# Performance work log

Measured on AMD Instinct MI355X. Metric: run time of the kernel, lower is better.

## Reference

```python
import jax, jax.numpy as jnp
import numpy as np

B, MBS, F, CD = 512, 32768, 512, 16  # batch, mini_batch_size, filter_length, cond_dim

def setup_inputs() -> dict:
    key = jax.random.key(0)
    ks = jax.random.split(key, 8)
    return {
        "inputs": jax.random.normal(ks[0], (B, MBS, 1), jnp.float32),
        "c": jax.random.normal(ks[1], (B, 1, CD), jnp.float32),
        "W0": jax.random.normal(ks[2], (CD, F), jnp.float32) * 0.1,
        "b0": jnp.zeros((F,), jnp.float32),
        "alpha": jnp.full((F,), 0.25, jnp.float32),
        "Wg": jax.random.normal(ks[3], (CD, F), jnp.float32) * 0.1,
        "bg": jnp.zeros((F,), jnp.float32),
        "Wb": jax.random.normal(ks[4], (CD, F), jnp.float32) * 0.1,
        "bb": jnp.zeros((F,), jnp.float32),
        "Wglu": jax.random.normal(ks[5], (F, 2 * F), jnp.float32) * 0.05,
        "bglu": jnp.zeros((2 * F,), jnp.float32),
        "Wf": jax.random.normal(ks[6], (F, F), jnp.float32) * 0.05,
        "bf": jnp.zeros((F,), jnp.float32),
    }

def reference(inputs, c, W0, b0, alpha, Wg, bg, Wb, bb, Wglu, bglu, Wf, bf):
    mbs = inputs.shape[1]
    flen = Wf.shape[1]
    # conditioning stack: Dense -> PReLU -> FiLM -> GLU -> Dense(softsign)
    c_ = c @ W0 + b0                                  # [B,1,F]
    c_ = jnp.where(c_ >= 0, c_, alpha * c_)           # PReLU
    c_ = c_ * (c @ Wg + bg) + (c @ Wb + bb)           # FiLM
    g = c_ @ Wglu + bglu                              # [B,1,2F]
    a, gate = jnp.split(g, 2, axis=-1)
    c_ = a * jax.nn.sigmoid(gate)                     # GLU
    filters = jax.nn.soft_sign(c_ @ Wf + bf)          # [B,1,F]
    # FFT-based circular (linear via zero pad) convolution
    conv_len = mbs + flen - 1
    X = jnp.fft.fft(inputs[:, :, 0].astype(jnp.complex64), n=conv_len)   # [B,conv_len]
    H = jnp.fft.fft(filters[:, 0, :].astype(jnp.complex64), n=conv_len)  # [B,conv_len]
    y = jnp.fft.ifft(X * H)
    return jnp.real(y[:, :mbs])                       # [B,MBS]
```

## Files before the change

### kernel.cpp

```cpp
#include <hip/hip_runtime.h>


typedef float f32x16 __attribute__((ext_vector_type(16)));
typedef float f32x4  __attribute__((ext_vector_type(4)));
typedef __bf16 bf16x8 __attribute__((ext_vector_type(8)));

__device__ __forceinline__ unsigned short f2bf(float f) {
    unsigned int u = __float_as_uint(f);
    u += 0x7FFFu + ((u >> 16) & 1u);
    return (unsigned short)(u >> 16);
}

__device__ __forceinline__ uint4 pack8n(float4 a, float4 b) {
    bf16x8 v;
    v[0] = (__bf16)a.x; v[1] = (__bf16)a.y; v[2] = (__bf16)a.z; v[3] = (__bf16)a.w;
    v[4] = (__bf16)b.x; v[5] = (__bf16)b.y; v[6] = (__bf16)b.z; v[7] = (__bf16)b.w;
    uint4 r;
    __builtin_memcpy(&r, &v, 16);
    return r;
}

__global__ __launch_bounds__(256) void kA(
    const float* __restrict__ Wglu, const float* __restrict__ Wf,
    const float* __restrict__ c, const float* __restrict__ W0,
    const float* __restrict__ b0, const float* __restrict__ alpha,
    const float* __restrict__ Wg, const float* __restrict__ bg,
    const float* __restrict__ Wb, const float* __restrict__ bb,
    unsigned short* __restrict__ WgluT, unsigned short* __restrict__ WfT,
    unsigned short* __restrict__ cfilm) {
    const int blk = blockIdx.x, tid = threadIdx.x;
    if (blk < 192) {
        __shared__ float ldsF[64 * 65];
        const float* src; unsigned short* dst; int tj, tk, srcld;
        if (blk < 128) { tj = blk >> 3; tk = blk & 7; src = Wglu; dst = WgluT; srcld = 1024; }
        else { int b2 = blk - 128; tj = b2 >> 3; tk = b2 & 7; src = Wf; dst = WfT; srcld = 512; }
#pragma unroll
        for (int rr = 0; rr < 16; ++rr) {
            int kl = (tid >> 6) + (rr << 2), jl = tid & 63;
            ldsF[kl * 65 + jl] = src[(size_t)(tk * 64 + kl) * srcld + tj * 64 + jl];
        }
        __syncthreads();
#pragma unroll
        for (int rr = 0; rr < 16; ++rr) {
            int jl = (tid >> 6) + (rr << 2), kl = tid & 63;
            dst[(size_t)(tj * 64 + jl) * 512 + tk * 64 + kl] = f2bf(ldsF[kl * 65 + jl]);
        }
    } else {
        int id = (blk - 192) * 256 + tid;
        int b = id >> 9, f = id & 511;
        const float* cb = c + b * 16;
        float d0 = 0.f, dg = 0.f, db = 0.f;
#pragma unroll
        for (int i = 0; i < 16; ++i) {
            float cv = cb[i];
            d0 += cv * W0[i * 512 + f];
            dg += cv * Wg[i * 512 + f];
            db += cv * Wb[i * 512 + f];
        }
        float pre = d0 + b0[f];
        float pr = pre >= 0.f ? pre : alpha[f] * pre;
        float v = pr * (dg + bg[f]) + (db + bb[f]);
        cfilm[id] = f2bf(v);
    }
}

__global__ __launch_bounds__(256) void k2_glu(
    const unsigned short* __restrict__ cfilm, const unsigned short* __restrict__ WgluT,
    const float* __restrict__ bglu, unsigned short* __restrict__ cglu) {
    int wid = (blockIdx.x * 256 + threadIdx.x) >> 6;
    int l = threadIdx.x & 63;
    int tm = wid >> 5, tn = wid & 31;
    int row = tm * 16 + (l & 15);
    int col = tn * 16 + (l & 15);
    int kh = 8 * (l >> 4);
    f32x4 accA, accG;
#pragma unroll
    for (int i = 0; i < 4; ++i) { accA[i] = 0.f; accG[i] = 0.f; }
    const unsigned short* ap  = cfilm + row * 512 + kh;
    const unsigned short* bap = WgluT + col * 512 + kh;
    const unsigned short* bgp = WgluT + (512 + col) * 512 + kh;
#pragma unroll
    for (int kc = 0; kc < 16; ++kc) {
        bf16x8 a   = *(const bf16x8*)(ap  + kc * 32);
        bf16x8 ba  = *(const bf16x8*)(bap + kc * 32);
        bf16x8 bgt = *(const bf16x8*)(bgp + kc * 32);
        accA = __builtin_amdgcn_mfma_f32_16x16x32_bf16(a, ba,  accA, 0, 0, 0);
        accG = __builtin_amdgcn_mfma_f32_16x16x32_bf16(a, bgt, accG, 0, 0, 0);
    }
    float biasA = bglu[col], biasG = bglu[512 + col];
#pragma unroll
    for (int r = 0; r < 4; ++r) {
        float ga = accA[r] + biasA;
        float gg = accG[r] + biasG;
        float s = 1.f / (1.f + expf(-gg));
        int m = (l >> 4) * 4 + r;
        cglu[(tm * 16 + m) * 512 + col] = f2bf(ga * s);
    }
}

__global__ __launch_bounds__(256) void k3_filt(
    const unsigned short* __restrict__ cglu, const unsigned short* __restrict__ WfT,
    const float* __restrict__ bfv, unsigned short* __restrict__ hout) {
    int wid = (blockIdx.x * 256 + threadIdx.x) >> 6;
    int l = threadIdx.x & 63;
    int tm = wid >> 5, tn = wid & 31;
    int row = tm * 16 + (l & 15);
    int col = tn * 16 + (l & 15);
    int kh = 8 * (l >> 4);
    f32x4 acc;
#pragma unroll
    for (int i = 0; i < 4; ++i) acc[i] = 0.f;
    const unsigned short* ap = cglu + row * 512 + kh;
    const unsigned short* bp = WfT + col * 512 + kh;
#pragma unroll
    for (int kc = 0; kc < 16; ++kc) {
        bf16x8 a  = *(const bf16x8*)(ap + kc * 32);
        bf16x8 bv = *(const bf16x8*)(bp + kc * 32);
        acc = __builtin_amdgcn_mfma_f32_16x16x32_bf16(a, bv, acc, 0, 0, 0);
    }
    float bias = bfv[col];
#pragma unroll
    for (int r = 0; r < 4; ++r) {
        float z = acc[r] + bias;
        float h = z / (1.f + fabsf(z));
        int m = (l >> 4) * 4 + r;
        hout[(tm * 16 + m) * 512 + col] = f2bf(h);
    }
}

__global__ __launch_bounds__(256, 2) void k5e(
    const float* __restrict__ x, const unsigned short* __restrict__ hbf,
    float* __restrict__ y) {
    __shared__ __align__(16) unsigned char smem[45184];
    const int tid = threadIdx.x;
    const int b = blockIdx.x;
    const float* xb = x + (size_t)b * 32768;
    unsigned short* hs = (unsigned short*)(smem + 44160);

    ((unsigned int*)hs)[tid] = ((const unsigned int*)(hbf + (size_t)b * 512))[tid];
    __syncthreads();

    for (int e = tid; e < 8 * 292; e += 256) {
        int s = e / 292, w = e - s * 292;
        int j0 = 2 * w + s;
        unsigned int v0 = (j0 >= 32 && j0 < 544) ? hs[543 - j0] : 0u;
        unsigned int v1 = (j0 >= 31 && j0 < 543) ? hs[542 - j0] : 0u;
        ((unsigned int*)(smem + 34816))[e] = v0 | (v1 << 16);
    }

#pragma unroll
    for (int r = 0; r < 5; ++r) {
        int slot = tid + (r << 8);
        if (slot < 1088) {
            int g = slot - 64;
            uint4 w4;
            if (g >= 0) {
                float4 a  = *(const float4*)(xb + g * 8);
                float4 b2 = *(const float4*)(xb + g * 8 + 4);
                w4 = pack8n(a, b2);
            } else {
                w4 = make_uint4(0u, 0u, 0u, 0u);
            }
            *(uint4*)(smem + ((slot ^ ((slot >> 3) & 7)) << 4)) = w4;
        }
    }
    __syncthreads();

    const int w = tid >> 6, l = tid & 63;
    const int q = l & 31, hl = l >> 5;
    const int lq = 4 * q + hl;
    const int abase = 66 + (w << 8) + lq;
    const int o0 = 559 - q + 8 * hl;
    const int s8 = o0 & 7;
    const unsigned char* hrb = smem + 34816 + s8 * 1168 + ((o0 - s8) << 1);

    for (int c = 0; c < 4; ++c) {
        const unsigned char* wb = smem + ((c & 1) ? 17408 : 0);
        unsigned char* sb = smem + ((c & 1) ? 0 : 17408);
        float4 La0, La1, La2, La3, La4, Lb0, Lb1, Lb2, Lb3, Lb4;
        if (c < 3) {
            const float* px = xb + (((c + 1) << 13) - 512);
            La0 = *(const float4*)(px + (tid << 3));           Lb0 = *(const float4*)(px + (tid << 3) + 4);
            La1 = *(const float4*)(px + ((tid + 256) << 3));   Lb1 = *(const float4*)(px + ((tid + 256) << 3) + 4);
            La2 = *(const float4*)(px + ((tid + 512) << 3));   Lb2 = *(const float4*)(px + ((tid + 512) << 3) + 4);
            La3 = *(const float4*)(px + ((tid + 768) << 3));   Lb3 = *(const float4*)(px + ((tid + 768) << 3) + 4);
            if (tid < 64) {
                La4 = *(const float4*)(px + ((tid + 1024) << 3));
                Lb4 = *(const float4*)(px + ((tid + 1024) << 3) + 4);
            }
        }
        f32x16 acc0, acc1;
#pragma unroll
        for (int i = 0; i < 16; ++i) { acc0[i] = 0.f; acc1[i] = 0.f; }
#pragma unroll
        for (int cc = 0; cc < 17; ++cc) {
            bf16x8 bfr = *(const bf16x8*)(hrb - (cc << 5));
            int a0 = abase - 2 * cc, a1 = a0 + 128;
            bf16x8 xa0 = *(const bf16x8*)(wb + ((a0 ^ ((a0 >> 3) & 7)) << 4));
            bf16x8 xa1 = *(const bf16x8*)(wb + ((a1 ^ ((a1 >> 3) & 7)) << 4));
            acc0 = __builtin_amdgcn_mfma_f32_32x32x16_bf16(xa0, bfr, acc0, 0, 0, 0);
            acc1 = __builtin_amdgcn_mfma_f32_32x32x16_bf16(xa1, bfr, acc1, 0, 0, 0);
        }
#pragma unroll
        for (int cc = 17; cc < 34; ++cc) {
            bf16x8 bfr = *(const bf16x8*)(hrb - (cc << 5));
            int a0 = abase - 2 * cc, a1 = a0 + 128;
            bf16x8 xa0 = *(const bf16x8*)(wb + ((a0 ^ ((a0 >> 3) & 7)) << 4));
            bf16x8 xa1 = *(const bf16x8*)(wb + ((a1 ^ ((a1 >> 3) & 7)) << 4));
            acc0 = __builtin_amdgcn_mfma_f32_32x32x16_bf16(xa0, bfr, acc0, 0, 0, 0);
            acc1 = __builtin_amdgcn_mfma_f32_32x32x16_bf16(xa1, bfr, acc1, 0, 0, 0);
        }
        if (c < 3) {
            int s0 = tid;
            *(uint4*)(sb + ((s0 ^ ((s0 >> 3) & 7)) << 4)) = pack8n(La0, Lb0);
            int s1 = tid + 256;
            *(uint4*)(sb + ((s1 ^ ((s1 >> 3) & 7)) << 4)) = pack8n(La1, Lb1);
            int s2 = tid + 512;
            *(uint4*)(sb + ((s2 ^ ((s2 >> 3) & 7)) << 4)) = pack8n(La2, Lb2);
            int s3 = tid + 768;
            *(uint4*)(sb + ((s3 ^ ((s3 >> 3) & 7)) << 4)) = pack8n(La3, Lb3);
            if (tid < 64) {
                int s4 = tid + 1024;
                *(uint4*)(sb + ((s4 ^ ((s4 >> 3) & 7)) << 4)) = pack8n(La4, Lb4);
            }
        }
        asm volatile("s_waitcnt lgkmcnt(0)" ::: "memory");
        __builtin_amdgcn_s_barrier();
        __builtin_amdgcn_sched_barrier(0);
        float* yb = y + (size_t)b * 32768 + (c << 13) + (w << 11) + q;
#pragma unroll
        for (int r = 0; r < 16; ++r) {
            int m = (r & 3) + 8 * (r >> 2) + 4 * hl;
            yb[m << 5] = acc0[r];
            yb[1024 + (m << 5)] = acc1[r];
        }
    }
}

extern "C" void kernel_launch(void* const* d_in, const int* in_sizes, int n_in,
                              void* d_out, int out_size, void* d_ws, size_t ws_size,
                              hipStream_t stream) {
    const float* x    = (const float*)d_in[0];
    const float* c    = (const float*)d_in[1];
    const float* W0   = (const float*)d_in[2];
    const float* b0   = (const float*)d_in[3];
    const float* al   = (const float*)d_in[4];
    const float* Wg   = (const float*)d_in[5];
    const float* bg   = (const float*)d_in[6];
    const float* Wb   = (const float*)d_in[7];
    const float* bb   = (const float*)d_in[8];
    const float* Wglu = (const float*)d_in[9];
    const float* bglu = (const float*)d_in[10];
    const float* Wf   = (const float*)d_in[11];
    const float* bf   = (const float*)d_in[12];
    float* y = (float*)d_out;

    char* ws = (char*)d_ws;
    unsigned short* cfilm = (unsigned short*)(ws);
    unsigned short* WgluT = (unsigned short*)(ws + 524288);
    unsigned short* WfT   = (unsigned short*)(ws + 1572864);
    unsigned short* cglu  = (unsigned short*)(ws + 2097152);
    unsigned short* hbf   = (unsigned short*)(ws + 2621440);

    kA<<<dim3(1216), dim3(256), 0, stream>>>(Wglu, Wf, c, W0, b0, al, Wg, bg, Wb, bb,
                                             WgluT, WfT, cfilm);
    k2_glu<<<dim3(256), dim3(256), 0, stream>>>(cfilm, WgluT, bglu, cglu);
    k3_filt<<<dim3(256), dim3(256), 0, stream>>>(cglu, WfT, bf, hbf);
    k5e<<<dim3(512), dim3(256), 0, stream>>>(x, hbf, y);
}
```

Baseline: 49.18 us.

## Pre-convert input to swizzled bf16 and stream it into LDS via global_load_lds

Adds a pass in the first kernel that converts the signal x to bf16, zero-pads it and stores it in the swizzled workspace layout. A new convolution kernel then pulls windows directly into LDS with global_load_lds, skipping the register round trip and the in-kernel pack. The goal is to cut register pressure and VALU pack work in the main MFMA loop while halving the bytes the main kernel reads. In exchange it adds an extra global write and read of the converted signal (about 34 MB of workspace). It falls back to the old kernel when the workspace is too small.

Result: slower. 59.49 us (+21.0%).

```diff
diff --git a/kernel.cpp b/kernel.cpp
--- a/kernel.cpp
+++ b/kernel.cpp
@@ -20,14 +20,21 @@
     return r;
 }
 
+__device__ __forceinline__ void gl_lds16(const void* g, void* l) {
+    __builtin_amdgcn_global_load_lds(
+        (const __attribute__((address_space(1))) unsigned int*)g,
+        (__attribute__((address_space(3))) unsigned int*)l, 16, 0, 0);
+}
+
 __global__ __launch_bounds__(256) void kA(
     const float* __restrict__ Wglu, const float* __restrict__ Wf,
     const float* __restrict__ c, const float* __restrict__ W0,
     const float* __restrict__ b0, const float* __restrict__ alpha,
     const float* __restrict__ Wg, const float* __restrict__ bg,
     const float* __restrict__ Wb, const float* __restrict__ bb,
+    const float* __restrict__ x,
     unsigned short* __restrict__ WgluT, unsigned short* __restrict__ WfT,
-    unsigned short* __restrict__ cfilm) {
+    unsigned short* __restrict__ cfilm, unsigned short* __restrict__ xswz) {
     const int blk = blockIdx.x, tid = threadIdx.x;
     if (blk < 192) {
         __shared__ float ldsF[64 * 65];
@@ -45,7 +52,7 @@
             int jl = (tid >> 6) + (rr << 2), kl = tid & 63;
             dst[(size_t)(tj * 64 + jl) * 512 + tk * 64 + kl] = f2bf(ldsF[kl * 65 + jl]);
         }
-    } else {
+    } else if (blk < 1216) {
         int id = (blk - 192) * 256 + tid;
         int b = id >> 9, f = id & 511;
         const float* cb = c + b * 16;
@@ -61,6 +68,25 @@
         float pr = pre >= 0.f ? pre : alpha[f] * pre;
         float v = pr * (dg + bg[f]) + (db + bb[f]);
         cfilm[id] = f2bf(v);
+    } else {
+        int idx = blk - 1216;
+        int bb2 = idx >> 3, s = idx & 7;
+        const float* xb = x + (size_t)bb2 * 32768 + (s << 12);
+        unsigned short* dst = xswz + (size_t)bb2 * 33280;
+        float4 v0 = *(const float4*)(xb + (tid << 4));
+        float4 v1 = *(const float4*)(xb + (tid << 4) + 4);
+        float4 v2 = *(const float4*)(xb + (tid << 4) + 8);
+        float4 v3 = *(const float4*)(xb + (tid << 4) + 12);
+        int g0 = 64 + (s << 9) + (tid << 1);
+        int g1 = g0 + 1;
+        int su0 = g0 ^ ((g0 >> 3) & 7);
+        int su1 = g1 ^ ((g1 >> 3) & 7);
+        *(uint4*)(dst + (su0 << 3)) = pack8n(v0, v1);
+        *(uint4*)(dst + (su1 << 3)) = pack8n(v2, v3);
+        if (s == 0 && tid < 64) {
+            int su = tid ^ ((tid >> 3) & 7);
+            *(uint4*)(dst + (su << 3)) = make_uint4(0u, 0u, 0u, 0u);
+        }
     }
 }
 
@@ -128,6 +154,80 @@
     }
 }
 
+__global__ __launch_bounds__(256, 2) void k11(
+    const unsigned short* __restrict__ xswz, const unsigned short* __restrict__ hbf,
+    float* __restrict__ y) {
+    __shared__ __align__(16) unsigned char smem[45184];
+    const int tid = threadIdx.x;
+    const int b = blockIdx.x;
+    const unsigned short* xsb = xswz + (size_t)b * 33280;
+    unsigned short* hs = (unsigned short*)(smem + 44160);
+
+    ((unsigned int*)hs)[tid] = ((const unsigned int*)(hbf + (size_t)b * 512))[tid];
+    __syncthreads();
+
+    for (int e = tid; e < 8 * 292; e += 256) {
+        int s = e / 292, w2 = e - s * 292;
+        int j0 = 2 * w2 + s;
+        unsigned int v0 = (j0 >= 32 && j0 < 544) ? hs[543 - j0] : 0u;
+        unsigned int v1 = (j0 >= 31 && j0 < 543) ? hs[542 - j0] : 0u;
+        ((unsigned int*)(smem + 34816))[e] = v0 | (v1 << 16);
+    }
+
+    const int w = tid >> 6, l = tid & 63;
+#pragma unroll
+    for (int r = 0; r < 4; ++r) {
+        int ub = (r << 8) + (w << 6);
+        gl_lds16(xsb + ((ub + l) << 3), smem + (ub << 4));
+    }
+    if (w == 0) gl_lds16(xsb + ((1024 + l) << 3), smem + (1024 << 4));
+    __syncthreads();
+
+    const int q = l & 31, hl = l >> 5;
+    const int lq = 4 * q + hl;
+    const int abase = 66 + (w << 8) + lq;
+    const int o0 = 559 - q + 8 * hl;
+    const int s8 = o0 & 7;
+    const unsigned char* hrb = smem + 34816 + s8 * 1168 + ((o0 - s8) << 1);
+
+    for (int c = 0; c < 4; ++c) {
+        const unsigned char* wb = smem + ((c & 1) ? 17408 : 0);
+        unsigned char* sb = smem + ((c & 1) ? 0 : 17408);
+        if (c < 3) {
+            const unsigned short* win = xsb + (((c + 1) << 10) << 3);
+#pragma unroll
+            for (int r = 0; r < 4; ++r) {
+                int ub = (r << 8) + (w << 6);
+                gl_lds16(win + ((ub + l) << 3), sb + (ub << 4));
+            }
+            if (w == 0) gl_lds16(win + ((1024 + l) << 3), sb + (1024 << 4));
+            __builtin_amdgcn_sched_barrier(0);
+        }
+        f32x16 acc0, acc1;
+#pragma unroll
+        for (int i = 0; i < 16; ++i) { acc0[i] = 0.f; acc1[i] = 0.f; }
+#pragma unroll
+        for (int cc = 0; cc < 34; ++cc) {
+            bf16x8 bfr = *(const bf16x8*)(hrb - (cc << 5));
+            int a0 = abase - 2 * cc, a1 = a0 + 128;
+            bf16x8 xa0 = *(const bf16x8*)(wb + ((a0 ^ ((a0 >> 3) & 7)) << 4));
+            bf16x8 xa1 = *(const bf16x8*)(wb + ((a1 ^ ((a1 >> 3) & 7)) << 4));
+            acc0 = __builtin_amdgcn_mfma_f32_32x32x16_bf16(xa0, bfr, acc0, 0, 0, 0);
+            acc1 = __builtin_amdgcn_mfma_f32_32x32x16_bf16(xa1, bfr, acc1, 0, 0, 0);
+        }
+        asm volatile("s_waitcnt vmcnt(0)" ::: "memory");
+        __builtin_amdgcn_s_barrier();
+        __builtin_amdgcn_sched_barrier(0);
+        float* yb = y + (size_t)b * 32768 + (c << 13) + (w << 11) + q;
+#pragma unroll
+        for (int r = 0; r < 16; ++r) {
+            int m = (r & 3) + 8 * (r >> 2) + 4 * hl;
+            yb[m << 5] = acc0[r];
+            yb[1024 + (m << 5)] = acc1[r];
+        }
+    }
+}
+
 __global__ __launch_bounds__(256, 2) void k5e(
     const float* __restrict__ x, const unsigned short* __restrict__ hbf,
     float* __restrict__ y) {
@@ -139,15 +239,13 @@
 
     ((unsigned int*)hs)[tid] = ((const unsigned int*)(hbf + (size_t)b * 512))[tid];
     __syncthreads();
-
     for (int e = tid; e < 8 * 292; e += 256) {
-        int s = e / 292, w = e - s * 292;
-        int j0 = 2 * w + s;
+        int s = e / 292, w2 = e - s * 292;
+        int j0 = 2 * w2 + s;
         unsigned int v0 = (j0 >= 32 && j0 < 544) ? hs[543 - j0] : 0u;
         unsigned int v1 = (j0 >= 31 && j0 < 543) ? hs[542 - j0] : 0u;
         ((unsigned int*)(smem + 34816))[e] = v0 | (v1 << 16);
     }
-
 #pragma unroll
     for (int r = 0; r < 5; ++r) {
         int slot = tid + (r << 8);
@@ -193,16 +291,7 @@
 #pragma unroll
         for (int i = 0; i < 16; ++i) { acc0[i] = 0.f; acc1[i] = 0.f; }
 #pragma unroll
-        for (int cc = 0; cc < 17; ++cc) {
-            bf16x8 bfr = *(const bf16x8*)(hrb - (cc << 5));
-            int a0 = abase - 2 * cc, a1 = a0 + 128;
-            bf16x8 xa0 = *(const bf16x8*)(wb + ((a0 ^ ((a0 >> 3) & 7)) << 4));
-            bf16x8 xa1 = *(const bf16x8*)(wb + ((a1 ^ ((a1 >> 3) & 7)) << 4));
-            acc0 = __builtin_amdgcn_mfma_f32_32x32x16_bf16(xa0, bfr, acc0, 0, 0, 0);
-            acc1 = __builtin_amdgcn_mfma_f32_32x32x16_bf16(xa1, bfr, acc1, 0, 0, 0);
-        }
-#pragma unroll
-        for (int cc = 17; cc < 34; ++cc) {
+        for (int cc = 0; cc < 34; ++cc) {
             bf16x8 bfr = *(const bf16x8*)(hrb - (cc << 5));
             int a0 = abase - 2 * cc, a1 = a0 + 128;
             bf16x8 xa0 = *(const bf16x8*)(wb + ((a0 ^ ((a0 >> 3) & 7)) << 4));
@@ -261,10 +350,17 @@
     unsigned short* WfT   = (unsigned short*)(ws + 1572864);
     unsigned short* cglu  = (unsigned short*)(ws + 2097152);
     unsigned short* hbf   = (unsigned short*)(ws + 2621440);
-
-    kA<<<dim3(1216), dim3(256), 0, stream>>>(Wglu, Wf, c, W0, b0, al, Wg, bg, Wb, bb,
-                                             WgluT, WfT, cfilm);
+    unsigned short* xswz  = (unsigned short*)(ws + 3145728);
+
+    const bool big = ws_size >= (size_t)(3145728 + 512 * 66560);
+
+    kA<<<dim3(big ? 5312 : 1216), dim3(256), 0, stream>>>(
+        Wglu, Wf, c, W0, b0, al, Wg, bg, Wb, bb, x, WgluT, WfT, cfilm, xswz);
     k2_glu<<<dim3(256), dim3(256), 0, stream>>>(cfilm, WgluT, bglu, cglu);
     k3_filt<<<dim3(256), dim3(256), 0, stream>>>(cglu, WfT, bf, hbf);
-    k5e<<<dim3(512), dim3(256), 0, stream>>>(x, hbf, y);
-}
+    if (big) {
+        k11<<<dim3(512), dim3(256), 0, stream>>>(xswz, hbf, y);
+    } else {
+        k5e<<<dim3(512), dim3(256), 0, stream>>>(x, hbf, y);
+    }
+}
```

## Split each batch row across two blocks and raise occupancy to three

Applied to the files above, without the earlier changes.

The convolution kernel now launches two blocks per batch row, each handling half of the output samples (two chunks instead of four), with the halo taken from the preceding input region. Launch bounds are raised to allow three resident blocks per CU, and the inner MFMA loop is merged into a single 34-step unrolled loop. The aim is better CU coverage and latency hiding on a grid that was otherwise only 512 blocks. The trade-off is that filter preparation and the initial halo load are repeated per block, and register pressure may rise.

After: 55.43 us. 12.7% more time.

```diff
diff --git a/kernel.cpp b/kernel.cpp
--- a/kernel.cpp
+++ b/kernel.cpp
@@ -128,12 +128,13 @@
     }
 }
 
-__global__ __launch_bounds__(256, 2) void k5e(
+__global__ __launch_bounds__(256, 3) void k12(
     const float* __restrict__ x, const unsigned short* __restrict__ hbf,
     float* __restrict__ y) {
     __shared__ __align__(16) unsigned char smem[45184];
     const int tid = threadIdx.x;
-    const int b = blockIdx.x;
+    const int b = blockIdx.x >> 1;
+    const int n0 = (blockIdx.x & 1) << 14;
     const float* xb = x + (size_t)b * 32768;
     unsigned short* hs = (unsigned short*)(smem + 44160);
 
@@ -141,8 +142,8 @@
     __syncthreads();
 
     for (int e = tid; e < 8 * 292; e += 256) {
-        int s = e / 292, w = e - s * 292;
-        int j0 = 2 * w + s;
+        int s = e / 292, w2 = e - s * 292;
+        int j0 = 2 * w2 + s;
         unsigned int v0 = (j0 >= 32 && j0 < 544) ? hs[543 - j0] : 0u;
         unsigned int v1 = (j0 >= 31 && j0 < 543) ? hs[542 - j0] : 0u;
         ((unsigned int*)(smem + 34816))[e] = v0 | (v1 << 16);
@@ -152,11 +153,11 @@
     for (int r = 0; r < 5; ++r) {
         int slot = tid + (r << 8);
         if (slot < 1088) {
-            int g = slot - 64;
+            int off = n0 + ((slot - 64) << 3);
             uint4 w4;
-            if (g >= 0) {
-                float4 a  = *(const float4*)(xb + g * 8);
-                float4 b2 = *(const float4*)(xb + g * 8 + 4);
+            if (off >= 0) {
+                float4 a  = *(const float4*)(xb + off);
+                float4 b2 = *(const float4*)(xb + off + 4);
                 w4 = pack8n(a, b2);
             } else {
                 w4 = make_uint4(0u, 0u, 0u, 0u);
@@ -174,12 +175,13 @@
     const int s8 = o0 & 7;
     const unsigned char* hrb = smem + 34816 + s8 * 1168 + ((o0 - s8) << 1);
 
-    for (int c = 0; c < 4; ++c) {
+#pragma unroll
+    for (int c = 0; c < 2; ++c) {
         const unsigned char* wb = smem + ((c & 1) ? 17408 : 0);
         unsigned char* sb = smem + ((c & 1) ? 0 : 17408);
         float4 La0, La1, La2, La3, La4, Lb0, Lb1, Lb2, Lb3, Lb4;
-        if (c < 3) {
-            const float* px = xb + (((c + 1) << 13) - 512);
+        if (c < 1) {
+            const float* px = xb + n0 + (1 << 13) - 512;
             La0 = *(const float4*)(px + (tid << 3));           Lb0 = *(const float4*)(px + (tid << 3) + 4);
             La1 = *(const float4*)(px + ((tid + 256) << 3));   Lb1 = *(const float4*)(px + ((tid + 256) << 3) + 4);
             La2 = *(const float4*)(px + ((tid + 512) << 3));   Lb2 = *(const float4*)(px + ((tid + 512) << 3) + 4);
@@ -193,7 +195,7 @@
 #pragma unroll
         for (int i = 0; i < 16; ++i) { acc0[i] = 0.f; acc1[i] = 0.f; }
 #pragma unroll
-        for (int cc = 0; cc < 17; ++cc) {
+        for (int cc = 0; cc < 34; ++cc) {
             bf16x8 bfr = *(const bf16x8*)(hrb - (cc << 5));
             int a0 = abase - 2 * cc, a1 = a0 + 128;
             bf16x8 xa0 = *(const bf16x8*)(wb + ((a0 ^ ((a0 >> 3) & 7)) << 4));
@@ -201,16 +203,7 @@
             acc0 = __builtin_amdgcn_mfma_f32_32x32x16_bf16(xa0, bfr, acc0, 0, 0, 0);
             acc1 = __builtin_amdgcn_mfma_f32_32x32x16_bf16(xa1, bfr, acc1, 0, 0, 0);
         }
-#pragma unroll
-        for (int cc = 17; cc < 34; ++cc) {
-            bf16x8 bfr = *(const bf16x8*)(hrb - (cc << 5));
-            int a0 = abase - 2 * cc, a1 = a0 + 128;
-            bf16x8 xa0 = *(const bf16x8*)(wb + ((a0 ^ ((a0 >> 3) & 7)) << 4));
-            bf16x8 xa1 = *(const bf16x8*)(wb + ((a1 ^ ((a1 >> 3) & 7)) << 4));
-            acc0 = __builtin_amdgcn_mfma_f32_32x32x16_bf16(xa0, bfr, acc0, 0, 0, 0);
-            acc1 = __builtin_amdgcn_mfma_f32_32x32x16_bf16(xa1, bfr, acc1, 0, 0, 0);
-        }
-        if (c < 3) {
+        if (c < 1) {
             int s0 = tid;
             *(uint4*)(sb + ((s0 ^ ((s0 >> 3) & 7)) << 4)) = pack8n(La0, Lb0);
             int s1 = tid + 256;
@@ -227,7 +220,7 @@
         asm volatile("s_waitcnt lgkmcnt(0)" ::: "memory");
         __builtin_amdgcn_s_barrier();
         __builtin_amdgcn_sched_barrier(0);
-        float* yb = y + (size_t)b * 32768 + (c << 13) + (w << 11) + q;
+        float* yb = y + (size_t)b * 32768 + n0 + (c << 13) + (w << 11) + q;
 #pragma unroll
         for (int r = 0; r < 16; ++r) {
             int m = (r & 3) + 8 * (r >> 2) + 4 * hl;
@@ -266,5 +259,5 @@
                                              WgluT, WfT, cfilm);
     k2_glu<<<dim3(256), dim3(256), 0, stream>>>(cfilm, WgluT, bglu, cglu);
     k3_filt<<<dim3(256), dim3(256), 0, stream>>>(cglu, WfT, bf, hbf);
-    k5e<<<dim3(512), dim3(256), 0, stream>>>(x, hbf, y);
-}
+    k12<<<dim3(1024), dim3(256), 0, stream>>>(x, hbf, y);
+}
```
